# Performance work log

Measured on AMD Instinct MI355X. Metric: run time of the kernel, lower is better.

## Reference

```python
import jax, jax.numpy as jnp
import numpy as np

EPS = 1e-6

def layer_norm(x, g, b):
    mu = jnp.mean(x, axis=-1, keepdims=True)
    var = jnp.mean((x - mu) ** 2, axis=-1, keepdims=True)
    return (x - mu) / jnp.sqrt(var + EPS) * g + b

def mha(q, k, v, Wq, bq, Wk, bk, Wv, bv, Wo, bo, nhead):
    B, Lq, D = q.shape
    Lk = k.shape[1]
    dh = D // nhead
    Q = (q @ Wq + bq).reshape(B, Lq, nhead, dh).transpose(0, 2, 1, 3)
    K = (k @ Wk + bk).reshape(B, Lk, nhead, dh).transpose(0, 2, 1, 3)
    V = (v @ Wv + bv).reshape(B, Lk, nhead, dh).transpose(0, 2, 1, 3)
    scores = jnp.einsum('bhqd,bhkd->bhqk', Q, K) / jnp.sqrt(jnp.asarray(dh, Q.dtype))
    attn = jax.nn.softmax(scores, axis=-1)
    out = jnp.einsum('bhqk,bhkd->bhqd', attn, V)
    out = out.transpose(0, 2, 1, 3).reshape(B, Lq, D)
    return out @ Wo + bo

def setup_inputs():
    key = jax.random.key(0)
    B, Lq, Lkv, D, F = 2, 1024, 4096, 512, 2048
    ks = jax.random.split(key, 32)
    s = 0.02
    inp = {
        'hidden_states':    jax.random.normal(ks[0], (B, Lq, D), jnp.float32),
        'hidden_states_pe': jax.random.normal(ks[1], (B, Lq, D), jnp.float32),
        'frame_states':     jax.random.normal(ks[2], (B, Lkv, D), jnp.float32),
        'frame_states_pe':  jax.random.normal(ks[3], (B, Lkv, D), jnp.float32),
        'obj_states':       jax.random.normal(ks[4], (B, Lkv, D), jnp.float32),
        'obj_states_pe':    jax.random.normal(ks[5], (B, Lkv, D), jnp.float32),
    }
    i = 6
    for p in ('f', 'o'):
        for w in ('Wq', 'Wk', 'Wv', 'Wo'):
            inp[f'{p}_{w}'] = jax.random.normal(ks[i], (D, D), jnp.float32) * s; i += 1
        for b in ('bq', 'bk', 'bv', 'bo'):
            inp[f'{p}_{b}'] = jnp.zeros((D,), jnp.float32)
        inp[f'{p}_g'] = jnp.ones((D,), jnp.float32)
        inp[f'{p}_b'] = jnp.zeros((D,), jnp.float32)
    inp['ffn_W1'] = jax.random.normal(ks[i], (D, F), jnp.float32) * s; i += 1
    inp['ffn_b1'] = jnp.zeros((F,), jnp.float32)
    inp['ffn_W2'] = jax.random.normal(ks[i], (F, D), jnp.float32) * s; i += 1
    inp['ffn_b2'] = jnp.zeros((D,), jnp.float32)
    inp['n3_g'] = jnp.ones((D,), jnp.float32)
    inp['n3_b'] = jnp.zeros((D,), jnp.float32)
    return inp

def reference(hidden_states, hidden_states_pe, frame_states, frame_states_pe,
              obj_states, obj_states_pe,
              f_Wq, f_Wk, f_Wv, f_Wo, f_bq, f_bk, f_bv, f_bo, f_g, f_b,
              o_Wq, o_Wk, o_Wv, o_Wo, o_bq, o_bk, o_bv, o_bo, o_g, o_b,
              ffn_W1, ffn_b1, ffn_W2, ffn_b2, n3_g, n3_b):
    nhead = 8
    x = hidden_states
    # frame memory cross-attention sublayer (pre-LN residual)
    q = layer_norm(x, f_g, f_b) + hidden_states_pe
    x = x + mha(q, frame_states + frame_states_pe, frame_states,
                f_Wq, f_bq, f_Wk, f_bk, f_Wv, f_bv, f_Wo, f_bo, nhead)
    # object memory cross-attention sublayer
    q = layer_norm(x, o_g, o_b) + hidden_states_pe
    x = x + mha(q, obj_states + obj_states_pe, obj_states,
                o_Wq, o_bq, o_Wk, o_bk, o_Wv, o_bv, o_Wo, o_bo, nhead)
    # FFN sublayer
    h = layer_norm(x, n3_g, n3_b)
    x = x + (jax.nn.relu(h @ ffn_W1 + ffn_b1) @ ffn_W2 + ffn_b2)
    return (x, frame_states, obj_states)
```

## Files before the change

### kernel.cpp

```cpp
#include <hip/hip_runtime.h>

typedef __attribute__((ext_vector_type(8))) short bf16x8;
typedef __attribute__((ext_vector_type(4))) short bf16x4;
typedef __attribute__((ext_vector_type(4))) float f32x4;
typedef __attribute__((ext_vector_type(4))) unsigned int u32x4;

#define DEV static __device__ __forceinline__

DEV short f2bf(float f) {
  union { float f; unsigned u; } v; v.f = f;
  unsigned r = v.u + 0x7fffu + ((v.u >> 16) & 1u);
  return (short)(r >> 16);
}
DEV unsigned pack2(float lo, float hi) {
  return ((unsigned)(unsigned short)f2bf(hi) << 16) | (unsigned)(unsigned short)f2bf(lo);
}

DEV void gload16(const void* g, void* l) {
  __builtin_amdgcn_global_load_lds(
      (const __attribute__((address_space(1))) unsigned int*)g,
      (__attribute__((address_space(3))) unsigned int*)l, 16, 0, 0);
}

DEV void ttile(const float* __restrict__ W, short* __restrict__ Wt, int K, int N,
               int k0, int n0, float (*t)[65], int tid) {
  const int c = tid & 63, r4 = tid >> 6;
#pragma unroll
  for (int i = 0; i < 16; i++)
    t[i * 4 + r4][c] = W[(size_t)(k0 + i * 4 + r4) * N + n0 + c];
  __syncthreads();
#pragma unroll
  for (int i = 0; i < 16; i++)
    Wt[(size_t)(n0 + i * 4 + r4) * K + k0 + c] = f2bf(t[c][i * 4 + r4]);
}

struct Tc8 { const float* src[8]; short* dst[8]; };

__global__ __launch_bounds__(256)
void tcast_tile8_kernel(Tc8 a) {
  __shared__ float t[64][65];
  ttile(a.src[blockIdx.z], a.dst[blockIdx.z], 512, 512,
        blockIdx.x * 64, blockIdx.y * 64, t, threadIdx.x);
}

__global__ __launch_bounds__(256)
void tcast_tile_kernel(const float* __restrict__ W, short* __restrict__ Wt, int K, int N) {
  __shared__ float t[64][65];
  ttile(W, Wt, K, N, blockIdx.x * 64, blockIdx.y * 64, t, threadIdx.x);
}

__global__ __launch_bounds__(256)
void addpe_kernel(const float* __restrict__ a, const float* __restrict__ p,
                  short* __restrict__ outK, short* __restrict__ outV) {
  size_t i = (size_t)(blockIdx.x * 256 + threadIdx.x) * 4;
  f32x4 va = *(const f32x4*)(a + i);
  f32x4 vp = *(const f32x4*)(p + i);
  bf16x4 k, v;
#pragma unroll
  for (int j = 0; j < 4; j++) { k[j] = f2bf(va[j] + vp[j]); v[j] = f2bf(va[j]); }
  *(bf16x4*)(outK + i) = k;
  *(bf16x4*)(outV + i) = v;
}

template<int PE>
__global__ __launch_bounds__(256)
void ln_kernel(const float* __restrict__ X, const float* __restrict__ gamma,
               const float* __restrict__ beta, const float* __restrict__ pe,
               short* __restrict__ Y) {
  const int wave = threadIdx.x >> 6, lane = threadIdx.x & 63;
  const int row = blockIdx.x * 4 + wave;
  const float* x = X + (size_t)row * 512 + lane * 8;
  f32x4 v0 = *(const f32x4*)x;
  f32x4 v1 = *(const f32x4*)(x + 4);
  float s = ((v0[0] + v0[1]) + (v0[2] + v0[3])) + ((v1[0] + v1[1]) + (v1[2] + v1[3]));
#pragma unroll
  for (int m = 1; m < 64; m <<= 1) s += __shfl_xor(s, m);
  float mu = s * (1.0f / 512.0f);
  float vs = 0.0f;
#pragma unroll
  for (int j = 0; j < 4; j++) { float d = v0[j] - mu; vs += d * d; }
#pragma unroll
  for (int j = 0; j < 4; j++) { float d = v1[j] - mu; vs += d * d; }
#pragma unroll
  for (int m = 1; m < 64; m <<= 1) vs += __shfl_xor(vs, m);
  float rstd = rsqrtf(vs * (1.0f / 512.0f) + 1e-6f);
  const int c = lane * 8;
  f32x4 g0 = *(const f32x4*)(gamma + c);
  f32x4 g1 = *(const f32x4*)(gamma + c + 4);
  f32x4 b0 = *(const f32x4*)(beta + c);
  f32x4 b1 = *(const f32x4*)(beta + c + 4);
  f32x4 p0 = {0,0,0,0}, p1 = {0,0,0,0};
  if (PE) {
    p0 = *(const f32x4*)(pe + (size_t)row * 512 + c);
    p1 = *(const f32x4*)(pe + (size_t)row * 512 + c + 4);
  }
  bf16x8 out;
#pragma unroll
  for (int j = 0; j < 4; j++) out[j]     = f2bf((v0[j] - mu) * rstd * g0[j] + b0[j] + p0[j]);
#pragma unroll
  for (int j = 0; j < 4; j++) out[4 + j] = f2bf((v1[j] - mu) * rstd * g1[j] + b1[j] + p1[j]);
  *(bf16x8*)(Y + (size_t)row * 512 + c) = out;
}

template<int FM, int FN, int OUTMODE, int RELU>
__global__ __launch_bounds__(256)
void gemm2_kernel(const short* __restrict__ A, const short* __restrict__ Bt,
                  const float* __restrict__ bias, const float* __restrict__ res,
                  void* __restrict__ Cv, int M, int N, int Klen, int lda, int ldb) {
  constexpr int BM = 32 * FM, BN = 32 * FN;
  __shared__ alignas(16) short As[2][BM * 32];
  __shared__ alignas(16) short Bs[2][BN * 32];
  const int tid = threadIdx.x;
  const int lane = tid & 63, w = tid >> 6;
  const int g = lane >> 4, x15 = lane & 15;
  const int wm = w >> 1, wn = w & 1;
  const int Mb = blockIdx.x * BM, Nb = blockIdx.y * BN;
  const short* Ag = A + (size_t)Mb * lda;
  const short* Bg = Bt + (size_t)Nb * ldb;

  auto stage = [&](int kb, int cur) {
    const int c = tid & 3, rr = tid >> 2;
#pragma unroll
    for (int j = 0; j < BM / 64; j++) {
      int row = j * 64 + rr;
      gload16(Ag + (size_t)row * lda + kb + ((c ^ (row & 3)) << 3),
              &As[cur][j * 2048 + tid * 8]);
    }
#pragma unroll
    for (int j = 0; j < BN / 64; j++) {
      int row = j * 64 + rr;
      gload16(Bg + (size_t)row * ldb + kb + ((c ^ (row & 3)) << 3),
              &Bs[cur][j * 2048 + tid * 8]);
    }
  };

  f32x4 acc[FM][FN] = {};
  const int nt = Klen >> 5;
  stage(0, 0);
  __syncthreads();
  int cur = 0;
  for (int t = 0; t < nt; t++) {
    if (t + 1 < nt) stage((t + 1) << 5, cur ^ 1);
    const char* Ac = (const char*)&As[cur][0];
    const char* Bc = (const char*)&Bs[cur][0];
    const int swr = (g ^ (x15 & 3)) << 4;
    bf16x8 af[FM], bfr[FN];
#pragma unroll
    for (int fm = 0; fm < FM; fm++)
      af[fm] = *(const bf16x8*)(Ac + (wm * (BM / 2) + fm * 16 + x15) * 64 + swr);
#pragma unroll
    for (int fn = 0; fn < FN; fn++)
      bfr[fn] = *(const bf16x8*)(Bc + (wn * (BN / 2) + fn * 16 + x15) * 64 + swr);
#pragma unroll
    for (int fm = 0; fm < FM; fm++)
#pragma unroll
      for (int fn = 0; fn < FN; fn++)
        acc[fm][fn] = __builtin_amdgcn_mfma_f32_16x16x32_bf16(af[fm], bfr[fn], acc[fm][fn], 0, 0, 0);
    __syncthreads();
    cur ^= 1;
  }

#pragma unroll
  for (int fm = 0; fm < FM; fm++)
#pragma unroll
    for (int fn = 0; fn < FN; fn++) {
      int n = Nb + wn * (BN / 2) + fn * 16 + x15;
      float bs = bias[n];
      int m0 = Mb + wm * (BM / 2) + fm * 16 + g * 4;
      if (OUTMODE == 2) {
        int bh = ((m0 >> 12) << 3) + (n >> 6);
        bf16x4 ov;
#pragma unroll
        for (int r = 0; r < 4; r++) ov[r] = f2bf(acc[fm][fn][r] + bs);
        *(bf16x4*)((short*)Cv + ((size_t)bh * 64 + (n & 63)) * 4096 + (m0 & 4095)) = ov;
      } else {
#pragma unroll
        for (int r = 0; r < 4; r++) {
          int m = m0 + r;
          float v = acc[fm][fn][r] + bs;
          if (RELU) v = fmaxf(v, 0.0f);
          if (OUTMODE == 1) {
            ((float*)Cv)[(size_t)m * N + n] = res[(size_t)m * N + n] + v;
          } else {
            ((short*)Cv)[(size_t)m * N + n] = f2bf(v);
          }
        }
      }
    }
}

__global__ __launch_bounds__(256, 4)
void attn_kernel(const short* __restrict__ Q, const short* __restrict__ K,
                 const short* __restrict__ Vt, float* __restrict__ Opart,
                 float2* __restrict__ ml) {
  __shared__ alignas(16) short Kl[2][4096];
  __shared__ alignas(16) short Vl[2][4096];

  const int tid = threadIdx.x;
  const int lane = tid & 63, w = tid >> 6;
  const int g = lane >> 4, q = lane & 15;
  const int o = (blockIdx.x & 7) * 128 + (blockIdx.x >> 3);
  const int ks = o >> 8, bh = (o >> 4) & 15, qtg = o & 15;
  const int b = bh >> 3, h = bh & 7;
  const int qt = qtg * 4 + w;

  const char* Kg = (const char*)K + ((size_t)b * 4096 * 512 + h * 64) * 2;
  const char* Vg = (const char*)Vt + ((size_t)bh * 64 * 4096) * 2;
  const int swz = (((lane & 7) ^ (lane >> 3)) << 4);
  const int sw = (q & 7) << 4;

  const short* Qp = Q + ((size_t)b * 1024 + qt * 16) * 512 + h * 64;
  bf16x8 qf0 = *(const bf16x8*)(Qp + (size_t)q * 512 + g * 8);
  bf16x8 qf1 = *(const bf16x8*)(Qp + (size_t)q * 512 + 32 + g * 8);

  f32x4 acc[4] = {{0,0,0,0},{0,0,0,0},{0,0,0,0},{0,0,0,0}};
  float mrun = -1e30f, lsum = 0.0f;
  const int k0 = ks * 1024;
  const int r0 = w * 16;

  auto stage = [&](int kb, int cur) {
    const char* kg = Kg + (size_t)(kb + r0 + (lane >> 3)) * 1024 + swz;
    gload16(kg,            &Kl[cur][r0 * 64]);
    gload16(kg + 8 * 1024, &Kl[cur][(r0 + 8) * 64]);
    const char* vg = Vg + (size_t)(r0 + (lane >> 3)) * 8192 + (size_t)kb * 2 + swz;
    gload16(vg,            &Vl[cur][r0 * 64]);
    gload16(vg + 8 * 8192, &Vl[cur][(r0 + 8) * 64]);
  };

  stage(k0, 0);
  __syncthreads();
  int cur = 0;
  for (int t = 0; t < 16; t++) {
    if (t < 15) stage(k0 + (t + 1) * 64, cur ^ 1);
    const char* Kc = (const char*)&Kl[cur][0];
    const char* Vc = (const char*)&Vl[cur][0];
#pragma unroll
    for (int ks32 = 0; ks32 < 2; ks32++) {
      const char* Kb8 = Kc + ks32 * 4096;
      bf16x8 k00 = *(const bf16x8*)(Kb8 + q * 128        + ((g * 16) ^ sw));
      bf16x8 k01 = *(const bf16x8*)(Kb8 + q * 128        + ((64 + g * 16) ^ sw));
      bf16x8 k10 = *(const bf16x8*)(Kb8 + (q + 16) * 128 + ((g * 16) ^ sw));
      bf16x8 k11 = *(const bf16x8*)(Kb8 + (q + 16) * 128 + ((64 + g * 16) ^ sw));
      f32x4 s0 = {0,0,0,0}, s1 = {0,0,0,0};
      __builtin_amdgcn_s_setprio(1);
      s0 = __builtin_amdgcn_mfma_f32_16x16x32_bf16(k00, qf0, s0, 0, 0, 0);
      s0 = __builtin_amdgcn_mfma_f32_16x16x32_bf16(k01, qf1, s0, 0, 0, 0);
      s1 = __builtin_amdgcn_mfma_f32_16x16x32_bf16(k10, qf0, s1, 0, 0, 0);
      s1 = __builtin_amdgcn_mfma_f32_16x16x32_bf16(k11, qf1, s1, 0, 0, 0);
      __builtin_amdgcn_s_setprio(0);

      float sv[8];
      float tmax = -1e30f;
#pragma unroll
      for (int r = 0; r < 4; r++) { sv[r] = s0[r] * 0.125f; tmax = fmaxf(tmax, sv[r]); }
#pragma unroll
      for (int r = 0; r < 4; r++) { sv[4 + r] = s1[r] * 0.125f; tmax = fmaxf(tmax, sv[4 + r]); }
      tmax = fmaxf(tmax, __shfl_xor(tmax, 16));
      tmax = fmaxf(tmax, __shfl_xor(tmax, 32));

      if (__any(tmax > mrun + 6.0f)) {
        float mnew = fmaxf(mrun, tmax);
        float corr = __expf(mrun - mnew);
        lsum *= corr;
#pragma unroll
        for (int df = 0; df < 4; df++)
#pragma unroll
          for (int r = 0; r < 4; r++) acc[df][r] *= corr;
        mrun = mnew;
      }
      float p[8], psum = 0.0f;
#pragma unroll
      for (int i = 0; i < 8; i++) { p[i] = __expf(sv[i] - mrun); psum += p[i]; }
      psum += __shfl_xor(psum, 16);
      psum += __shfl_xor(psum, 32);
      lsum += psum;

      unsigned w00 = pack2(p[0], p[1]), w01 = pack2(p[2], p[3]);
      unsigned w10 = pack2(p[4], p[5]), w11 = pack2(p[6], p[7]);
      int src0 = (g & 1) * 32 + q;
      int src1 = src0 + 16;
      unsigned a0 = (unsigned)__shfl((int)w00, src0);
      unsigned a1 = (unsigned)__shfl((int)w01, src0);
      unsigned c0 = (unsigned)__shfl((int)w10, src0);
      unsigned c1 = (unsigned)__shfl((int)w11, src0);
      unsigned d0 = (unsigned)__shfl((int)w00, src1);
      unsigned d1 = (unsigned)__shfl((int)w01, src1);
      unsigned e0 = (unsigned)__shfl((int)w10, src1);
      unsigned e1 = (unsigned)__shfl((int)w11, src1);
      int fsel = g >> 1;
      u32x4 pw;
      pw[0] = fsel ? c0 : a0;
      pw[1] = fsel ? c1 : a1;
      pw[2] = fsel ? e0 : d0;
      pw[3] = fsel ? e1 : d1;
      bf16x8 pfrag = __builtin_bit_cast(bf16x8, pw);

      __builtin_amdgcn_s_setprio(1);
#pragma unroll
      for (int df = 0; df < 4; df++) {
        bf16x8 vf = *(const bf16x8*)(Vc + (df * 16 + q) * 128 + ((ks32 * 64 + g * 16) ^ sw));
        acc[df] = __builtin_amdgcn_mfma_f32_16x16x32_bf16(vf, pfrag, acc[df], 0, 0, 0);
      }
      __builtin_amdgcn_s_setprio(0);
    }
    __syncthreads();
    cur ^= 1;
  }

  const int row = bh * 1024 + qt * 16 + q;
  float* Op = Opart + ((size_t)ks * 16384 + row) * 64 + g * 4;
#pragma unroll
  for (int df = 0; df < 4; df++) *(f32x4*)(Op + df * 16) = acc[df];
  if (g == 0) ml[(size_t)ks * 16384 + row] = make_float2(mrun, lsum);
}

__global__ __launch_bounds__(256)
void attn_combine_kernel(const float* __restrict__ Opart, const float2* __restrict__ ml,
                         short* __restrict__ attnb) {
  const int qt = blockIdx.x;
  const int bh = blockIdx.y;
  const int q = threadIdx.x >> 4, dq = threadIdx.x & 15;
  const int row = bh * 1024 + qt * 16 + q;
  float2 m0 = ml[row];
  float2 m1 = ml[16384 + row];
  float2 m2 = ml[2 * 16384 + row];
  float2 m3 = ml[3 * 16384 + row];
  float M = fmaxf(fmaxf(m0.x, m1.x), fmaxf(m2.x, m3.x));
  float e0 = __expf(m0.x - M), e1 = __expf(m1.x - M);
  float e2 = __expf(m2.x - M), e3 = __expf(m3.x - M);
  float inv = 1.0f / (m0.y * e0 + m1.y * e1 + m2.y * e2 + m3.y * e3);
  const size_t base = (size_t)row * 64 + dq * 4;
  f32x4 a0 = *(const f32x4*)(Opart + base);
  f32x4 a1 = *(const f32x4*)(Opart + (size_t)16384 * 64 + base);
  f32x4 a2 = *(const f32x4*)(Opart + (size_t)2 * 16384 * 64 + base);
  f32x4 a3 = *(const f32x4*)(Opart + (size_t)3 * 16384 * 64 + base);
  bf16x4 oo;
#pragma unroll
  for (int j = 0; j < 4; j++)
    oo[j] = f2bf((a0[j] * e0 + a1[j] * e1 + a2[j] * e2 + a3[j] * e3) * inv);
  const int b = bh >> 3, h = bh & 7;
  *(bf16x4*)(attnb + ((size_t)b * 1024 + qt * 16 + q) * 512 + h * 64 + dq * 4) = oo;
}

extern "C" void kernel_launch(void* const* d_in, const int* in_sizes, int n_in,
                              void* d_out, int out_size, void* d_ws, size_t ws_size,
                              hipStream_t stream) {
  const int D = 512, F = 2048;
  const int Mq = 2048, Mkv = 8192;

  char* ws = (char*)d_ws;
  size_t off = 0;
  auto alloc = [&](size_t bytes) { char* p = ws + off; off += (bytes + 255) & ~(size_t)255; return p; };
  float* x    = (float*)alloc((size_t)Mq * D * 4);
  short* qln  = (short*)alloc((size_t)Mq * D * 2);
  short* kvK  = (short*)alloc((size_t)Mkv * D * 2);
  short* kvV  = (short*)alloc((size_t)Mkv * D * 2);
  short* Qb   = (short*)alloc((size_t)Mq * D * 2);
  short* Kb   = (short*)alloc((size_t)Mkv * D * 2);
  short* Vt   = (short*)alloc((size_t)Mkv * D * 2);
  short* attnb= (short*)alloc((size_t)Mq * D * 2);
  char*  big  = alloc((size_t)4 * 16384 * 64 * 4);
  float* Opart = (float*)big;
  short* hffn  = (short*)big;
  float2* mlb = (float2*)alloc((size_t)4 * 16384 * 8);
  short* WT[8];
  for (int i = 0; i < 8; i++) WT[i] = (short*)alloc((size_t)D * D * 2);
  short* w1T = (short*)alloc((size_t)D * F * 2);
  short* w2T = (short*)alloc((size_t)F * D * 2);

  Tc8 tc8;
  const int widx[8] = {6, 7, 8, 9, 16, 17, 18, 19};
  for (int i = 0; i < 8; i++) { tc8.src[i] = (const float*)d_in[widx[i]]; tc8.dst[i] = WT[i]; }
  tcast_tile8_kernel<<<dim3(8, 8, 8), 256, 0, stream>>>(tc8);
  tcast_tile_kernel<<<dim3(8, 32), 256, 0, stream>>>((const float*)d_in[26], w1T, 512, 2048);
  tcast_tile_kernel<<<dim3(32, 8), 256, 0, stream>>>((const float*)d_in[28], w2T, 2048, 512);

  float* out = (float*)d_out;
  hipMemcpyAsync(x, d_in[0], (size_t)Mq * D * 4, hipMemcpyDeviceToDevice, stream);
  hipMemcpyAsync(out + (size_t)Mq * D, d_in[2], (size_t)Mkv * D * 4, hipMemcpyDeviceToDevice, stream);
  hipMemcpyAsync(out + (size_t)Mq * D + (size_t)Mkv * D, d_in[4], (size_t)Mkv * D * 4,
                 hipMemcpyDeviceToDevice, stream);

  auto attn_sublayer = [&](int g_i, int b_i, int kv_i, int pe_i, int w0, int bq_i, int bk_i,
                           int bv_i, int bo_i) {
    ln_kernel<1><<<Mq / 4, 256, 0, stream>>>(x, (const float*)d_in[g_i], (const float*)d_in[b_i],
                                             (const float*)d_in[1], qln);
    addpe_kernel<<<(Mkv * D) / 1024, 256, 0, stream>>>((const float*)d_in[kv_i],
                                                       (const float*)d_in[pe_i], kvK, kvV);
    gemm2_kernel<2, 2, 0, 0><<<dim3(Mq / 64, D / 64), 256, 0, stream>>>(
        qln, WT[w0], (const float*)d_in[bq_i], nullptr, Qb, Mq, D, D, D, D);
    gemm2_kernel<4, 2, 0, 0><<<dim3(Mkv / 128, D / 64), 256, 0, stream>>>(
        kvK, WT[w0 + 1], (const float*)d_in[bk_i], nullptr, Kb, Mkv, D, D, D, D);
    gemm2_kernel<4, 2, 2, 0><<<dim3(Mkv / 128, D / 64), 256, 0, stream>>>(
        kvV, WT[w0 + 2], (const float*)d_in[bv_i], nullptr, Vt, Mkv, D, D, D, D);
    attn_kernel<<<1024, 256, 0, stream>>>(Qb, Kb, Vt, Opart, mlb);
    attn_combine_kernel<<<dim3(64, 16), 256, 0, stream>>>(Opart, mlb, attnb);
    gemm2_kernel<2, 2, 1, 0><<<dim3(Mq / 64, D / 64), 256, 0, stream>>>(
        attnb, WT[w0 + 3], (const float*)d_in[bo_i], x, x, Mq, D, D, D, D);
  };

  attn_sublayer(14, 15, 2, 3, 0, 10, 11, 12, 13);
  attn_sublayer(24, 25, 4, 5, 4, 20, 21, 22, 23);

  ln_kernel<0><<<Mq / 4, 256, 0, stream>>>(x, (const float*)d_in[30], (const float*)d_in[31],
                                           nullptr, qln);
  gemm2_kernel<4, 2, 0, 1><<<dim3(Mq / 128, F / 64), 256, 0, stream>>>(
      qln, w1T, (const float*)d_in[27], nullptr, hffn, Mq, F, D, D, D);
  gemm2_kernel<2, 2, 1, 0><<<dim3(Mq / 64, D / 64), 256, 0, stream>>>(
      hffn, w2T, (const float*)d_in[29], x, out, Mq, D, F, F, F);
}
```

Baseline: 434.4 us.

## Batch both sublayers' K/V projections, double attention split-K, enlarge GEMM tiles

The K/V add-PE and projection GEMMs for the frame and object memories are hoisted out of the sublayers. Each projection now runs as one merged GEMM over both memories, picking weights and bias per block half. The attention kernel splits the key range into 8 chunks of 512 instead of 4 of 1024, and the combine kernel reduces over 8 partials; this doubles the grid to fill the GPU better, at the cost of more partial-output traffic. The large GEMMs use 128x128 tiles, and the MFMA block is wrapped in s_setprio. The workspace is reorganised so the partial attention outputs alias the now-dead K/V input buffers.

```diff
diff --git a/kernel.cpp b/kernel.cpp
--- a/kernel.cpp
+++ b/kernel.cpp
@@ -102,10 +102,11 @@
   *(bf16x8*)(Y + (size_t)row * 512 + c) = out;
 }
 
-template<int FM, int FN, int OUTMODE, int RELU>
-__global__ __launch_bounds__(256)
-void gemm2_kernel(const short* __restrict__ A, const short* __restrict__ Bt,
-                  const float* __restrict__ bias, const float* __restrict__ res,
+template<int FM, int FN, int OUTMODE, int RELU, int MERGE>
+__global__ __launch_bounds__(256)
+void gemm3_kernel(const short* __restrict__ A, const short* __restrict__ Bt0,
+                  const short* __restrict__ Bt1, const float* __restrict__ bias0,
+                  const float* __restrict__ bias1, const float* __restrict__ res,
                   void* __restrict__ Cv, int M, int N, int Klen, int lda, int ldb) {
   constexpr int BM = 32 * FM, BN = 32 * FN;
   __shared__ alignas(16) short As[2][BM * 32];
@@ -115,6 +116,8 @@
   const int g = lane >> 4, x15 = lane & 15;
   const int wm = w >> 1, wn = w & 1;
   const int Mb = blockIdx.x * BM, Nb = blockIdx.y * BN;
+  const short* Bt = (MERGE && Mb >= (M >> 1)) ? Bt1 : Bt0;
+  const float* bias = (MERGE && Mb >= (M >> 1)) ? bias1 : bias0;
   const short* Ag = A + (size_t)Mb * lda;
   const short* Bg = Bt + (size_t)Nb * ldb;
 
@@ -151,11 +154,13 @@
 #pragma unroll
     for (int fn = 0; fn < FN; fn++)
       bfr[fn] = *(const bf16x8*)(Bc + (wn * (BN / 2) + fn * 16 + x15) * 64 + swr);
+    __builtin_amdgcn_s_setprio(1);
 #pragma unroll
     for (int fm = 0; fm < FM; fm++)
 #pragma unroll
       for (int fn = 0; fn < FN; fn++)
         acc[fm][fn] = __builtin_amdgcn_mfma_f32_16x16x32_bf16(af[fm], bfr[fn], acc[fm][fn], 0, 0, 0);
+    __builtin_amdgcn_s_setprio(0);
     __syncthreads();
     cur ^= 1;
   }
@@ -199,7 +204,7 @@
   const int tid = threadIdx.x;
   const int lane = tid & 63, w = tid >> 6;
   const int g = lane >> 4, q = lane & 15;
-  const int o = (blockIdx.x & 7) * 128 + (blockIdx.x >> 3);
+  const int o = ((blockIdx.x & 7) << 8) + (blockIdx.x >> 3);
   const int ks = o >> 8, bh = (o >> 4) & 15, qtg = o & 15;
   const int b = bh >> 3, h = bh & 7;
   const int qt = qtg * 4 + w;
@@ -215,7 +220,7 @@
 
   f32x4 acc[4] = {{0,0,0,0},{0,0,0,0},{0,0,0,0},{0,0,0,0}};
   float mrun = -1e30f, lsum = 0.0f;
-  const int k0 = ks * 1024;
+  const int k0 = ks * 512;
   const int r0 = w * 16;
 
   auto stage = [&](int kb, int cur) {
@@ -230,8 +235,8 @@
   stage(k0, 0);
   __syncthreads();
   int cur = 0;
-  for (int t = 0; t < 16; t++) {
-    if (t < 15) stage(k0 + (t + 1) * 64, cur ^ 1);
+  for (int t = 0; t < 8; t++) {
+    if (t < 7) stage(k0 + (t + 1) * 64, cur ^ 1);
     const char* Kc = (const char*)&Kl[cur][0];
     const char* Vc = (const char*)&Vl[cur][0];
 #pragma unroll
@@ -321,23 +326,25 @@
   const int bh = blockIdx.y;
   const int q = threadIdx.x >> 4, dq = threadIdx.x & 15;
   const int row = bh * 1024 + qt * 16 + q;
-  float2 m0 = ml[row];
-  float2 m1 = ml[16384 + row];
-  float2 m2 = ml[2 * 16384 + row];
-  float2 m3 = ml[3 * 16384 + row];
-  float M = fmaxf(fmaxf(m0.x, m1.x), fmaxf(m2.x, m3.x));
-  float e0 = __expf(m0.x - M), e1 = __expf(m1.x - M);
-  float e2 = __expf(m2.x - M), e3 = __expf(m3.x - M);
-  float inv = 1.0f / (m0.y * e0 + m1.y * e1 + m2.y * e2 + m3.y * e3);
+  float2 mls[8];
+  float M = -1e30f;
+#pragma unroll
+  for (int s = 0; s < 8; s++) { mls[s] = ml[(size_t)s * 16384 + row]; M = fmaxf(M, mls[s].x); }
+  float es[8], den = 0.0f;
+#pragma unroll
+  for (int s = 0; s < 8; s++) { es[s] = __expf(mls[s].x - M); den += mls[s].y * es[s]; }
+  float inv = 1.0f / den;
   const size_t base = (size_t)row * 64 + dq * 4;
-  f32x4 a0 = *(const f32x4*)(Opart + base);
-  f32x4 a1 = *(const f32x4*)(Opart + (size_t)16384 * 64 + base);
-  f32x4 a2 = *(const f32x4*)(Opart + (size_t)2 * 16384 * 64 + base);
-  f32x4 a3 = *(const f32x4*)(Opart + (size_t)3 * 16384 * 64 + base);
+  f32x4 accv = {0, 0, 0, 0};
+#pragma unroll
+  for (int s = 0; s < 8; s++) {
+    f32x4 a = *(const f32x4*)(Opart + (size_t)s * 16384 * 64 + base);
+#pragma unroll
+    for (int j = 0; j < 4; j++) accv[j] += a[j] * es[s];
+  }
   bf16x4 oo;
 #pragma unroll
-  for (int j = 0; j < 4; j++)
-    oo[j] = f2bf((a0[j] * e0 + a1[j] * e1 + a2[j] * e2 + a3[j] * e3) * inv);
+  for (int j = 0; j < 4; j++) oo[j] = f2bf(accv[j] * inv);
   const int b = bh >> 3, h = bh & 7;
   *(bf16x4*)(attnb + ((size_t)b * 1024 + qt * 16 + q) * 512 + h * 64 + dq * 4) = oo;
 }
@@ -346,23 +353,23 @@
                               void* d_out, int out_size, void* d_ws, size_t ws_size,
                               hipStream_t stream) {
   const int D = 512, F = 2048;
-  const int Mq = 2048, Mkv = 8192;
+  const int Mq = 2048, Mkv = 8192, Mkv2 = 16384;
 
   char* ws = (char*)d_ws;
   size_t off = 0;
   auto alloc = [&](size_t bytes) { char* p = ws + off; off += (bytes + 255) & ~(size_t)255; return p; };
+  char* kvbase = alloc((size_t)32 * 1024 * 1024);
+  short* kvK  = (short*)kvbase;
+  short* kvV  = (short*)(kvbase + (size_t)Mkv2 * D * 2);
+  float* Opart = (float*)kvbase;
+  short* hffn  = (short*)kvbase;
   float* x    = (float*)alloc((size_t)Mq * D * 4);
   short* qln  = (short*)alloc((size_t)Mq * D * 2);
-  short* kvK  = (short*)alloc((size_t)Mkv * D * 2);
-  short* kvV  = (short*)alloc((size_t)Mkv * D * 2);
   short* Qb   = (short*)alloc((size_t)Mq * D * 2);
-  short* Kb   = (short*)alloc((size_t)Mkv * D * 2);
-  short* Vt   = (short*)alloc((size_t)Mkv * D * 2);
+  short* Kb   = (short*)alloc((size_t)Mkv2 * D * 2);
+  short* Vt   = (short*)alloc((size_t)Mkv2 * D * 2);
   short* attnb= (short*)alloc((size_t)Mq * D * 2);
-  char*  big  = alloc((size_t)4 * 16384 * 64 * 4);
-  float* Opart = (float*)big;
-  short* hffn  = (short*)big;
-  float2* mlb = (float2*)alloc((size_t)4 * 16384 * 8);
+  float2* mlb = (float2*)alloc((size_t)8 * 16384 * 8);
   short* WT[8];
   for (int i = 0; i < 8; i++) WT[i] = (short*)alloc((size_t)D * D * 2);
   short* w1T = (short*)alloc((size_t)D * F * 2);
@@ -381,31 +388,36 @@
   hipMemcpyAsync(out + (size_t)Mq * D + (size_t)Mkv * D, d_in[4], (size_t)Mkv * D * 4,
                  hipMemcpyDeviceToDevice, stream);
 
-  auto attn_sublayer = [&](int g_i, int b_i, int kv_i, int pe_i, int w0, int bq_i, int bk_i,
-                           int bv_i, int bo_i) {
+  addpe_kernel<<<(Mkv * D) / 1024, 256, 0, stream>>>((const float*)d_in[2], (const float*)d_in[3],
+                                                     kvK, kvV);
+  addpe_kernel<<<(Mkv * D) / 1024, 256, 0, stream>>>((const float*)d_in[4], (const float*)d_in[5],
+                                                     kvK + (size_t)Mkv * D, kvV + (size_t)Mkv * D);
+  gemm3_kernel<4, 4, 0, 0, 1><<<dim3(Mkv2 / 128, D / 128), 256, 0, stream>>>(
+      kvK, WT[1], WT[5], (const float*)d_in[11], (const float*)d_in[21], nullptr,
+      Kb, Mkv2, D, D, D, D);
+  gemm3_kernel<4, 4, 2, 0, 1><<<dim3(Mkv2 / 128, D / 128), 256, 0, stream>>>(
+      kvV, WT[2], WT[6], (const float*)d_in[12], (const float*)d_in[22], nullptr,
+      Vt, Mkv2, D, D, D, D);
+
+  auto attn_sublayer = [&](int g_i, int b_i, int w0, int bq_i, int bo_i, int half) {
     ln_kernel<1><<<Mq / 4, 256, 0, stream>>>(x, (const float*)d_in[g_i], (const float*)d_in[b_i],
                                              (const float*)d_in[1], qln);
-    addpe_kernel<<<(Mkv * D) / 1024, 256, 0, stream>>>((const float*)d_in[kv_i],
-                                                       (const float*)d_in[pe_i], kvK, kvV);
-    gemm2_kernel<2, 2, 0, 0><<<dim3(Mq / 64, D / 64), 256, 0, stream>>>(
-        qln, WT[w0], (const float*)d_in[bq_i], nullptr, Qb, Mq, D, D, D, D);
-    gemm2_kernel<4, 2, 0, 0><<<dim3(Mkv / 128, D / 64), 256, 0, stream>>>(
-        kvK, WT[w0 + 1], (const float*)d_in[bk_i], nullptr, Kb, Mkv, D, D, D, D);
-    gemm2_kernel<4, 2, 2, 0><<<dim3(Mkv / 128, D / 64), 256, 0, stream>>>(
-        kvV, WT[w0 + 2], (const float*)d_in[bv_i], nullptr, Vt, Mkv, D, D, D, D);
-    attn_kernel<<<1024, 256, 0, stream>>>(Qb, Kb, Vt, Opart, mlb);
+    gemm3_kernel<2, 2, 0, 0, 0><<<dim3(Mq / 64, D / 64), 256, 0, stream>>>(
+        qln, WT[w0], nullptr, (const float*)d_in[bq_i], nullptr, nullptr, Qb, Mq, D, D, D, D);
+    attn_kernel<<<2048, 256, 0, stream>>>(Qb, Kb + (size_t)half * Mkv * D,
+                                          Vt + (size_t)half * 16 * 64 * 4096, Opart, mlb);
     attn_combine_kernel<<<dim3(64, 16), 256, 0, stream>>>(Opart, mlb, attnb);
-    gemm2_kernel<2, 2, 1, 0><<<dim3(Mq / 64, D / 64), 256, 0, stream>>>(
-        attnb, WT[w0 + 3], (const float*)d_in[bo_i], x, x, Mq, D, D, D, D);
+    gemm3_kernel<2, 2, 1, 0, 0><<<dim3(Mq / 64, D / 64), 256, 0, stream>>>(
+        attnb, WT[w0 + 3], nullptr, (const float*)d_in[bo_i], nullptr, x, x, Mq, D, D, D, D);
   };
 
-  attn_sublayer(14, 15, 2, 3, 0, 10, 11, 12, 13);
-  attn_sublayer(24, 25, 4, 5, 4, 20, 21, 22, 23);
+  attn_sublayer(14, 15, 0, 10, 13, 0);
+  attn_sublayer(24, 25, 4, 20, 23, 1);
 
   ln_kernel<0><<<Mq / 4, 256, 0, stream>>>(x, (const float*)d_in[30], (const float*)d_in[31],
                                            nullptr, qln);
-  gemm2_kernel<4, 2, 0, 1><<<dim3(Mq / 128, F / 64), 256, 0, stream>>>(
-      qln, w1T, (const float*)d_in[27], nullptr, hffn, Mq, F, D, D, D);
-  gemm2_kernel<2, 2, 1, 0><<<dim3(Mq / 64, D / 64), 256, 0, stream>>>(
-      hffn, w2T, (const float*)d_in[29], x, out, Mq, D, F, F, F);
-}
+  gemm3_kernel<4, 4, 0, 1, 0><<<dim3(Mq / 128, F / 128), 256, 0, stream>>>(
+      qln, w1T, nullptr, (const float*)d_in[27], nullptr, nullptr, hffn, Mq, F, D, D, D);
+  gemm3_kernel<2, 2, 1, 0, 0><<<dim3(Mq / 64, D / 64), 256, 0, stream>>>(
+      hffn, w2T, nullptr, (const float*)d_in[29], nullptr, x, out, Mq, D, F, F, F);
+}
```

Measured after the change: 431.4 us. About the same (-0.7%).
